# Kernel optimization log

Measured on AMD Instinct MI355X. Metric: run time of the kernel, lower is better.

Reference implementation:

```python
import jax, jax.numpy as jnp
import numpy as np

B = 128          # batch of trees (same topology)
N_LEAVES = 512
N_NODES = 2 * N_LEAVES - 1   # 1023, null child slot = N_NODES
IN_DIM = 300
MEM_DIM = 300


def _build_tree():
    # complete binary tree, level order: leaves first, then parents.
    null = N_NODES
    left = [null] * N_LEAVES
    right = [null] * N_LEAVES
    prev = list(range(N_LEAVES))
    nid = N_LEAVES
    while len(prev) > 1:
        cur = []
        for k in range(0, len(prev), 2):
            left.append(prev[k]); right.append(prev[k + 1])
            cur.append(nid); nid += 1
        prev = cur
    left = np.asarray(left, np.int32)
    right = np.asarray(right, np.int32)
    leaf_mask = (left == null).astype(np.int32)
    return left, right, leaf_mask


def setup_inputs() -> dict:
    key = jax.random.key(0)
    ks = jax.random.split(key, 5)
    left, right, leaf_mask = _build_tree()
    s = 0.05  # keep gates out of saturation
    return {
        "inputs": jax.random.normal(ks[0], (B, N_NODES, IN_DIM), jnp.float32),
        "Wfioux": jax.random.normal(ks[1], (IN_DIM, 4 * MEM_DIM), jnp.float32) * s,
        "b_fioux": jax.random.normal(ks[2], (4 * MEM_DIM,), jnp.float32) * s,
        "Wiouh": jax.random.normal(ks[3], (2 * MEM_DIM, 3 * MEM_DIM), jnp.float32) * s,
        "Wfh": jax.random.normal(ks[4], (2 * MEM_DIM, 2 * MEM_DIM), jnp.float32) * s,
        "left_idx": jnp.asarray(left),
        "right_idx": jnp.asarray(right),
        "leaf_mask": jnp.asarray(leaf_mask),
    }


def _tree_lstm(inputs, Wfioux, b_fioux, Wiouh, Wfh, left_idx, right_idx, leaf_mask):
    b, n, _ = inputs.shape
    mem = Wiouh.shape[1] // 3
    # internal nodes get zero input (as in the torch code)
    x = inputs * leaf_mask.astype(inputs.dtype)[None, :, None]
    # input-dependent gates precomputed for all nodes: [n, b, 4*mem]
    fioux = jnp.einsum('bni,io->nbo', x, Wfioux) + b_fioux

    C0 = jnp.zeros((n + 1, b, mem), inputs.dtype)  # row n = null child = zeros
    H0 = jnp.zeros((n + 1, b, mem), inputs.dtype)

    def step(carry, xs):
        C, H = carry
        i, li, ri, fioux_i = xs
        ch_c = jnp.concatenate([C[li], C[ri]], axis=-1)  # [b, 2*mem]
        ch_h = jnp.concatenate([H[li], H[ri]], axis=-1)
        fx, ix, ox, ux = jnp.split(fioux_i, 4, axis=-1)
        ih, oh, uh = jnp.split(ch_h @ Wiouh, 3, axis=-1)
        i_g = jax.nn.sigmoid(ix + ih)
        o_g = jax.nn.sigmoid(ox + oh)
        u_g = jnp.tanh(ux + uh)
        f_g = jax.nn.sigmoid(jnp.tile(fx, (1, 2)) + ch_h @ Wfh)
        fc = (f_g * ch_c).reshape(b, 2, mem).sum(axis=1)
        c = i_g * u_g + fc
        h = o_g * jnp.tanh(c)
        return (C.at[li * 0 + i].set(c), H.at[i].set(h)), None

    xs = (jnp.arange(n, dtype=jnp.int32), left_idx, right_idx, fioux)
    (C, H), _ = jax.lax.scan(step, (C0, H0), xs)
    return C[n - 1], H[n - 1]  # root state (c, h), each [b, mem]


def reference(inputs, Wfioux, b_fioux, Wiouh, Wfh, left_idx, right_idx, leaf_mask):
    return _tree_lstm(inputs, Wfioux, b_fioux, Wiouh, Wfh, left_idx, right_idx, leaf_mask)
```

## Files before the change

### kernel.cpp

```cpp
#include <hip/hip_runtime.h>
#include <cstdint>

#define BATCH 128
#define NODES 1023
#define LEAVES 512
#define IN_DIM 300
#define MEM 300
#define NP 320
#define OUT_HALF (BATCH*MEM)

typedef __bf16   bf16x8 __attribute__((ext_vector_type(8)));
typedef short    s16x8  __attribute__((ext_vector_type(8)));
typedef short    s16x4  __attribute__((ext_vector_type(4)));
typedef float    f32x4  __attribute__((ext_vector_type(4)));
typedef _Float16 half_t;

__device__ __forceinline__ short f2bf(float f) {
    unsigned u = __float_as_uint(f);
    u += 0x7fff + ((u >> 16) & 1);
    return (short)(u >> 16);
}
__device__ __forceinline__ float sigf(float x)  { return 1.0f / (1.0f + __expf(-x)); }
__device__ __forceinline__ float tanhf_(float x){ return 1.0f - 2.0f / (1.0f + __expf(2.0f * x)); }

__device__ __forceinline__ f32x4 mfma16(s16x8 a, s16x8 b, f32x4 c) {
    return __builtin_amdgcn_mfma_f32_16x16x32_bf16(
        __builtin_bit_cast(bf16x8, a), __builtin_bit_cast(bf16x8, b), c, 0, 0, 0);
}

__device__ __forceinline__ void dma16(const short* src, short* ldsBase) {
    __builtin_amdgcn_global_load_lds(
        (const __attribute__((address_space(1))) unsigned int*)src,
        (__attribute__((address_space(3))) unsigned int*)ldsBase,
        16, 0, 0);
}

__global__ __launch_bounds__(256) void pack_node_w(
    const float* __restrict__ Wiouh, const float* __restrict__ Wfh, short* __restrict__ Wpk)
{
    int gid = blockIdx.x * 256 + threadIdx.x;
    if (gid >= 2000 * 64) return;
    int fb = gid >> 6, l = gid & 63;
    int kb = fb / 100, rem = fb % 100, s = rem / 20, nb = rem % 20;
    int n = nb * 16 + (l & 15);
    int kbase = kb * 32 + (l >> 4) * 8;
    short v[8];
#pragma unroll
    for (int j = 0; j < 8; ++j) {
        int kp = kbase + j;
        int side = kp >= NP;
        int kk = kp - side * NP;
        float f = 0.0f;
        if (kk < MEM && n < MEM) {
            int k = side * MEM + kk;
            f = (s < 3) ? Wiouh[(size_t)k * 900 + s * 300 + n]
                        : Wfh[(size_t)k * 600 + (s - 3) * 300 + n];
        }
        v[j] = f2bf(f);
    }
    *(s16x8*)&Wpk[(size_t)gid * 8] = *(s16x8*)v;
}

__global__ __launch_bounds__(256) void pack_leaf_w(
    const float* __restrict__ Wfioux, short* __restrict__ Wpk)
{
    int gid = blockIdx.x * 256 + threadIdx.x;
    if (gid >= 600 * 64) return;
    int fb = gid >> 6, l = gid & 63;
    int kb = fb / 60, rem = fb % 60, s = rem / 20, nb = rem % 20;
    int n = nb * 16 + (l & 15);
    int kbase = kb * 32 + (l >> 4) * 8;
    short v[8];
#pragma unroll
    for (int j = 0; j < 8; ++j) {
        int kp = kbase + j;
        float f = 0.0f;
        if (kp < IN_DIM && n < MEM)
            f = Wfioux[(size_t)kp * 1200 + (s + 1) * 300 + n];
        v[j] = f2bf(f);
    }
    *(s16x8*)&Wpk[(size_t)gid * 8] = *(s16x8*)v;
}

__global__ __launch_bounds__(256) void pack_x(
    const float* __restrict__ inputs, short* __restrict__ X)
{
    int gid = blockIdx.x * 256 + threadIdx.x;
    if (gid >= LEAVES * BATCH * (NP / 4)) return;
    int q = gid % (NP / 4);
    int rb = gid / (NP / 4);
    int b = rb % BATCH, leaf = rb / BATCH;
    short v[4] = {0, 0, 0, 0};
    if (q < IN_DIM / 4) {
        f32x4 f = *(const f32x4*)&inputs[((size_t)b * NODES + leaf) * IN_DIM + q * 4];
        v[0] = f2bf(f[0]); v[1] = f2bf(f[1]); v[2] = f2bf(f[2]); v[3] = f2bf(f[3]);
    }
    *(s16x4*)&X[(size_t)gid * 4] = *(s16x4*)v;
}

__global__ __launch_bounds__(256, 3) void leaf_mfma(
    const short* __restrict__ X, const short* __restrict__ Wpk,
    const float* __restrict__ b_fioux, half_t* __restrict__ C, short* __restrict__ H)
{
    __shared__ short Bs[12 * 512];
    const int t = threadIdx.x;
    const int l = t & 63, w = t >> 6;
    const int lane16 = l & 15, quad = l >> 4;
    const int leaf = blockIdx.x;
    const int y = blockIdx.y;

    const short* Xb = X + (size_t)leaf * BATCH * NP;

    f32x4 acc[3][4][2];
#pragma unroll
    for (int s = 0; s < 3; ++s)
#pragma unroll
        for (int f = 0; f < 4; ++f)
#pragma unroll
            for (int mi = 0; mi < 2; ++mi) acc[s][f][mi] = (f32x4)(0.0f);

    for (int kb = 0; kb < 10; ++kb) {
        const int koff = kb * 32 + quad * 8;
#pragma unroll
        for (int fl = w; fl < 12; fl += 4) {
            int s = fl >> 2, f = fl & 3;
            const short* src = Wpk + ((size_t)((kb * 3 + s) * 20 + y * 4 + f) * 64 + l) * 8;
            dma16(src, &Bs[fl * 512]);
        }
        s16x8 a[2];
        a[0] = *(const s16x8*)(Xb + (size_t)(w * 32 + lane16) * NP + koff);
        a[1] = *(const s16x8*)(Xb + (size_t)(w * 32 + 16 + lane16) * NP + koff);
        __syncthreads();
#pragma unroll
        for (int s = 0; s < 3; ++s)
#pragma unroll
            for (int f = 0; f < 4; ++f) {
                s16x8 b = *(const s16x8*)&Bs[(s * 4 + f) * 512 + l * 8];
                acc[s][f][0] = mfma16(a[0], b, acc[s][f][0]);
                acc[s][f][1] = mfma16(a[1], b, acc[s][f][1]);
            }
        __syncthreads();
    }

#pragma unroll
    for (int f = 0; f < 4; ++f) {
        const int col = y * 64 + f * 16 + lane16;
        const bool valid = col < MEM;
        float bi = 0, bo = 0, bu = 0;
        if (valid) { bi = b_fioux[300 + col]; bo = b_fioux[600 + col]; bu = b_fioux[900 + col]; }
#pragma unroll
        for (int mi = 0; mi < 2; ++mi)
#pragma unroll
            for (int r = 0; r < 4; ++r) {
                int b = w * 32 + mi * 16 + quad * 4 + r;
                size_t hIdx = ((size_t)leaf * BATCH + b) * NP + col;
                if (valid) {
                    float ig = sigf(acc[0][f][mi][r] + bi);
                    float og = sigf(acc[1][f][mi][r] + bo);
                    float ug = tanhf_(acc[2][f][mi][r] + bu);
                    float c = ig * ug;
                    float h = og * tanhf_(c);
                    C[((size_t)leaf * BATCH + b) * MEM + col] = (half_t)c;
                    H[hIdx] = f2bf(h);
                } else {
                    H[hIdx] = 0;
                }
            }
    }
}

__global__ __launch_bounds__(256, 3) void node_mfma(
    const short* __restrict__ Wpk, const float* __restrict__ b_fioux,
    const int* __restrict__ left_idx, const int* __restrict__ right_idx,
    half_t* __restrict__ C, short* __restrict__ H,
    int level_start, float* __restrict__ out)
{
    __shared__ short Bs[10 * 512];
    const int t = threadIdx.x;
    const int l = t & 63, w = t >> 6;
    const int lane16 = l & 15, quad = l >> 4;
    const int node = level_start + blockIdx.x;
    const int y = blockIdx.y;

    const int li = left_idx[node], ri = right_idx[node];
    const short* HL = H + (size_t)li * BATCH * NP;
    const short* HR = H + (size_t)ri * BATCH * NP;

    f32x4 acc[5][2][2];
#pragma unroll
    for (int s = 0; s < 5; ++s)
#pragma unroll
        for (int f = 0; f < 2; ++f)
#pragma unroll
            for (int mi = 0; mi < 2; ++mi) acc[s][f][mi] = (f32x4)(0.0f);

    for (int kb = 0; kb < 20; ++kb) {
        const int side = kb >= 10;
        const int koff = (kb - side * 10) * 32 + quad * 8;
        const short* Hb = (side ? HR : HL) + koff;
#pragma unroll
        for (int fl = w; fl < 10; fl += 4) {
            int s = fl >> 1, f = fl & 1;
            const short* src = Wpk + ((size_t)((kb * 5 + s) * 20 + y * 2 + f) * 64 + l) * 8;
            dma16(src, &Bs[fl * 512]);
        }
        s16x8 a[2];
        a[0] = *(const s16x8*)(Hb + (size_t)(w * 32 + lane16) * NP);
        a[1] = *(const s16x8*)(Hb + (size_t)(w * 32 + 16 + lane16) * NP);
        __syncthreads();
#pragma unroll
        for (int s = 0; s < 5; ++s)
#pragma unroll
            for (int f = 0; f < 2; ++f) {
                s16x8 b = *(const s16x8*)&Bs[(s * 2 + f) * 512 + l * 8];
                acc[s][f][0] = mfma16(a[0], b, acc[s][f][0]);
                acc[s][f][1] = mfma16(a[1], b, acc[s][f][1]);
            }
        __syncthreads();
    }

#pragma unroll
    for (int f = 0; f < 2; ++f) {
        const int col = y * 32 + f * 16 + lane16;
        const bool valid = col < MEM;
        float bff = 0, bi = 0, bo = 0, bu = 0;
        if (valid) {
            bff = b_fioux[col]; bi = b_fioux[300 + col];
            bo = b_fioux[600 + col]; bu = b_fioux[900 + col];
        }
#pragma unroll
        for (int mi = 0; mi < 2; ++mi)
#pragma unroll
            for (int r = 0; r < 4; ++r) {
                int row = w * 32 + mi * 16 + quad * 4 + r;
                size_t hIdx = ((size_t)node * BATCH + row) * NP + col;
                if (valid) {
                    float cl = (float)C[((size_t)li * BATCH + row) * MEM + col];
                    float cr = (float)C[((size_t)ri * BATCH + row) * MEM + col];
                    float ig = sigf(acc[0][f][mi][r] + bi);
                    float og = sigf(acc[1][f][mi][r] + bo);
                    float ug = tanhf_(acc[2][f][mi][r] + bu);
                    float fl = sigf(acc[3][f][mi][r] + bff);
                    float fr = sigf(acc[4][f][mi][r] + bff);
                    float c = ig * ug + fl * cl + fr * cr;
                    float h = og * tanhf_(c);
                    C[((size_t)node * BATCH + row) * MEM + col] = (half_t)c;
                    H[hIdx] = f2bf(h);
                    if (out) {
                        out[row * MEM + col] = c;
                        out[OUT_HALF + row * MEM + col] = h;
                    }
                } else {
                    H[hIdx] = 0;
                }
            }
    }
}

extern "C" void kernel_launch(void* const* d_in, const int* in_sizes, int n_in,
                              void* d_out, int out_size, void* d_ws, size_t ws_size,
                              hipStream_t stream) {
    const float* inputs  = (const float*)d_in[0];
    const float* Wfioux  = (const float*)d_in[1];
    const float* b_fioux = (const float*)d_in[2];
    const float* Wiouh   = (const float*)d_in[3];
    const float* Wfh     = (const float*)d_in[4];
    const int*   left_idx  = (const int*)d_in[5];
    const int*   right_idx = (const int*)d_in[6];

    half_t* C   = (half_t*)d_ws;
    short*  H   = (short*)(C + (size_t)NODES * BATCH * MEM);
    short* WpkN = H + (size_t)NODES * BATCH * NP;
    short* WpkL = WpkN + (size_t)2000 * 512;
    short* X    = WpkL + (size_t)600 * 512;
    float* out  = (float*)d_out;

    pack_x<<<(LEAVES * BATCH * (NP / 4) + 255) / 256, 256, 0, stream>>>(inputs, X);
    pack_leaf_w<<<150, 256, 0, stream>>>(Wfioux, WpkL);
    pack_node_w<<<500, 256, 0, stream>>>(Wiouh, Wfh, WpkN);

    leaf_mfma<<<dim3(LEAVES, 5), 256, 0, stream>>>(X, WpkL, b_fioux, C, H);

    static const int starts[9] = {512, 768, 896, 960, 992, 1008, 1016, 1020, 1022};
    static const int sizes [9] = {256, 128,  64,  32,  16,    8,    4,    2,    1};
    for (int lvl = 0; lvl < 9; ++lvl) {
        bool root = (lvl == 8);
        node_mfma<<<dim3(sizes[lvl], 10), 256, 0, stream>>>(
            WpkN, b_fioux, left_idx, right_idx, C, H, starts[lvl],
            root ? out : nullptr);
    }
}
```

Before: 697.9 us.

## Double-buffer weight tiles and prefetch activations in leaf and node MFMA kernels

Both the leaf and internal-node GEMM kernels now ping-pong between two LDS buffers, issuing the DMA for the next K-block of packed weights and the register load of the next activation fragment before running the MFMAs on the current block. This removes one of the two barriers per iteration and overlaps global memory latency with matrix math. The node kernel also processes two 32-wide K sub-blocks per stage, halving the number of stages and barriers. The cost is more LDS (node kernel grows from 10 KB to 40 KB) and more live registers, which may cut occupancy under the 3-blocks launch bound.

```diff
diff --git a/kernel.cpp b/kernel.cpp
--- a/kernel.cpp
+++ b/kernel.cpp
@@ -102,7 +102,7 @@
     const short* __restrict__ X, const short* __restrict__ Wpk,
     const float* __restrict__ b_fioux, half_t* __restrict__ C, short* __restrict__ H)
 {
-    __shared__ short Bs[12 * 512];
+    __shared__ short Bs[2][12 * 512];
     const int t = threadIdx.x;
     const int l = t & 63, w = t >> 6;
     const int lane16 = l & 15, quad = l >> 4;
@@ -119,27 +119,39 @@
 #pragma unroll
             for (int mi = 0; mi < 2; ++mi) acc[s][f][mi] = (f32x4)(0.0f);
 
-    for (int kb = 0; kb < 10; ++kb) {
-        const int koff = kb * 32 + quad * 8;
+    auto stage = [&](int kb, int buf) {
 #pragma unroll
         for (int fl = w; fl < 12; fl += 4) {
             int s = fl >> 2, f = fl & 3;
             const short* src = Wpk + ((size_t)((kb * 3 + s) * 20 + y * 4 + f) * 64 + l) * 8;
-            dma16(src, &Bs[fl * 512]);
-        }
-        s16x8 a[2];
+            dma16(src, &Bs[buf][fl * 512]);
+        }
+    };
+    auto aload = [&](int kb, s16x8 (&a)[2]) {
+        const int koff = kb * 32 + quad * 8;
         a[0] = *(const s16x8*)(Xb + (size_t)(w * 32 + lane16) * NP + koff);
         a[1] = *(const s16x8*)(Xb + (size_t)(w * 32 + 16 + lane16) * NP + koff);
-        __syncthreads();
+    };
+
+    s16x8 aC[2], aN[2];
+    stage(0, 0);
+    aload(0, aC);
+    __syncthreads();
+
+#pragma unroll
+    for (int kb = 0; kb < 10; ++kb) {
+        const int buf = kb & 1;
+        if (kb < 9) { stage(kb + 1, buf ^ 1); aload(kb + 1, aN); }
 #pragma unroll
         for (int s = 0; s < 3; ++s)
 #pragma unroll
             for (int f = 0; f < 4; ++f) {
-                s16x8 b = *(const s16x8*)&Bs[(s * 4 + f) * 512 + l * 8];
-                acc[s][f][0] = mfma16(a[0], b, acc[s][f][0]);
-                acc[s][f][1] = mfma16(a[1], b, acc[s][f][1]);
+                s16x8 b = *(const s16x8*)&Bs[buf][(s * 4 + f) * 512 + l * 8];
+                acc[s][f][0] = mfma16(aC[0], b, acc[s][f][0]);
+                acc[s][f][1] = mfma16(aC[1], b, acc[s][f][1]);
             }
         __syncthreads();
+        aC[0] = aN[0]; aC[1] = aN[1];
     }
 
 #pragma unroll
@@ -175,7 +187,7 @@
     half_t* __restrict__ C, short* __restrict__ H,
     int level_start, float* __restrict__ out)
 {
-    __shared__ short Bs[10 * 512];
+    __shared__ short Bs[2][20 * 512];
     const int t = threadIdx.x;
     const int l = t & 63, w = t >> 6;
     const int lane16 = l & 15, quad = l >> 4;
@@ -194,29 +206,48 @@
 #pragma unroll
             for (int mi = 0; mi < 2; ++mi) acc[s][f][mi] = (f32x4)(0.0f);
 
-    for (int kb = 0; kb < 20; ++kb) {
-        const int side = kb >= 10;
-        const int koff = (kb - side * 10) * 32 + quad * 8;
-        const short* Hb = (side ? HR : HL) + koff;
-#pragma unroll
-        for (int fl = w; fl < 10; fl += 4) {
-            int s = fl >> 1, f = fl & 1;
-            const short* src = Wpk + ((size_t)((kb * 5 + s) * 20 + y * 2 + f) * 64 + l) * 8;
-            dma16(src, &Bs[fl * 512]);
-        }
-        s16x8 a[2];
-        a[0] = *(const s16x8*)(Hb + (size_t)(w * 32 + lane16) * NP);
-        a[1] = *(const s16x8*)(Hb + (size_t)(w * 32 + 16 + lane16) * NP);
+    auto stage = [&](int st, int buf) {
+#pragma unroll
+        for (int fl = w; fl < 20; fl += 4) {
+            int ksub = fl / 10, rem = fl - ksub * 10;
+            int s = rem >> 1, f = rem & 1;
+            int kb32 = st * 2 + ksub;
+            const short* src = Wpk + ((size_t)((kb32 * 5 + s) * 20 + y * 2 + f) * 64 + l) * 8;
+            dma16(src, &Bs[buf][fl * 512]);
+        }
+    };
+    auto aload = [&](int st, s16x8 (&a)[2][2]) {
+        const int side = st >= 5;
+        const short* Hb = (side ? HR : HL) + (st - side * 5) * 64 + quad * 8;
+#pragma unroll
+        for (int ksub = 0; ksub < 2; ++ksub) {
+            a[ksub][0] = *(const s16x8*)(Hb + (size_t)(w * 32 + lane16) * NP + ksub * 32);
+            a[ksub][1] = *(const s16x8*)(Hb + (size_t)(w * 32 + 16 + lane16) * NP + ksub * 32);
+        }
+    };
+
+    s16x8 aC[2][2], aN[2][2];
+    stage(0, 0);
+    aload(0, aC);
+    __syncthreads();
+
+#pragma unroll
+    for (int st = 0; st < 10; ++st) {
+        const int buf = st & 1;
+        if (st < 9) { stage(st + 1, buf ^ 1); aload(st + 1, aN); }
+#pragma unroll
+        for (int ksub = 0; ksub < 2; ++ksub)
+#pragma unroll
+            for (int s = 0; s < 5; ++s)
+#pragma unroll
+                for (int f = 0; f < 2; ++f) {
+                    s16x8 b = *(const s16x8*)&Bs[buf][(ksub * 10 + s * 2 + f) * 512 + l * 8];
+                    acc[s][f][0] = mfma16(aC[ksub][0], b, acc[s][f][0]);
+                    acc[s][f][1] = mfma16(aC[ksub][1], b, acc[s][f][1]);
+                }
         __syncthreads();
 #pragma unroll
-        for (int s = 0; s < 5; ++s)
-#pragma unroll
-            for (int f = 0; f < 2; ++f) {
-                s16x8 b = *(const s16x8*)&Bs[(s * 2 + f) * 512 + l * 8];
-                acc[s][f][0] = mfma16(a[0], b, acc[s][f][0]);
-                acc[s][f][1] = mfma16(a[1], b, acc[s][f][1]);
-            }
-        __syncthreads();
+        for (int i = 0; i < 2; ++i) { aC[i][0] = aN[i][0]; aC[i][1] = aN[i][1]; }
     }
 
 #pragma unroll
```

Measured after the change: 705.6 us. Within noise of the previous version (+1.1%).

## Software-pipeline K loop with 4-stage LDS ring and prefetch distance three

Applied to the files above, without the earlier changes.

Both the leaf and node MFMA kernels replace their synchronous per-k-block load/compute loop with a fully unrolled pipeline. It uses four LDS buffers and keeps weight DMAs and A-fragment loads three stages ahead, waiting with explicit vmcnt counts and a single barrier per step. The aim is to hide global-memory latency behind MFMA work instead of stalling on two barriers each iteration. In exchange it uses four times the shared memory (48KB per block) and more registers for the A fragments, which may cut occupancy under launch_bounds(256,3). The node kernel also pads its DMA to 12 slots so the vmcnt counts match, which adds duplicate loads. Dropping the trailing barrier relies on the 4-deep ring to avoid overwriting a buffer that is still being read.

```diff
diff --git a/kernel.cpp b/kernel.cpp
--- a/kernel.cpp
+++ b/kernel.cpp
@@ -102,7 +102,7 @@
     const short* __restrict__ X, const short* __restrict__ Wpk,
     const float* __restrict__ b_fioux, half_t* __restrict__ C, short* __restrict__ H)
 {
-    __shared__ short Bs[12 * 512];
+    __shared__ short Bs[4][12 * 512];
     const int t = threadIdx.x;
     const int l = t & 63, w = t >> 6;
     const int lane16 = l & 15, quad = l >> 4;
@@ -119,28 +119,49 @@
 #pragma unroll
             for (int mi = 0; mi < 2; ++mi) acc[s][f][mi] = (f32x4)(0.0f);
 
-    for (int kb = 0; kb < 10; ++kb) {
-        const int koff = kb * 32 + quad * 8;
-#pragma unroll
-        for (int fl = w; fl < 12; fl += 4) {
-            int s = fl >> 2, f = fl & 3;
-            const short* src = Wpk + ((size_t)((kb * 3 + s) * 20 + y * 4 + f) * 64 + l) * 8;
-            dma16(src, &Bs[fl * 512]);
-        }
-        s16x8 a[2];
-        a[0] = *(const s16x8*)(Xb + (size_t)(w * 32 + lane16) * NP + koff);
-        a[1] = *(const s16x8*)(Xb + (size_t)(w * 32 + 16 + lane16) * NP + koff);
-        __syncthreads();
-#pragma unroll
-        for (int s = 0; s < 3; ++s)
-#pragma unroll
-            for (int f = 0; f < 4; ++f) {
-                s16x8 b = *(const s16x8*)&Bs[(s * 4 + f) * 512 + l * 8];
-                acc[s][f][0] = mfma16(a[0], b, acc[s][f][0]);
-                acc[s][f][1] = mfma16(a[1], b, acc[s][f][1]);
-            }
-        __syncthreads();
-    }
+    s16x8 A[4][2];
+
+#define L_STAGE(KB, BUF) do {                                                    \
+    _Pragma("unroll")                                                            \
+    for (int fl = w; fl < 12; fl += 4) {                                         \
+        int s_ = fl >> 2, f_ = fl & 3;                                           \
+        const short* src_ = Wpk +                                                \
+            ((size_t)(((KB) * 3 + s_) * 20 + y * 4 + f_) * 64 + l) * 8;          \
+        dma16(src_, &Bs[BUF][fl * 512]);                                         \
+    } } while (0)
+
+#define L_ALOAD(KB, SLOT) do {                                                   \
+    const int koff_ = (KB) * 32 + quad * 8;                                      \
+    A[SLOT][0] = *(const s16x8*)(Xb + (size_t)(w * 32 + lane16) * NP + koff_);   \
+    A[SLOT][1] = *(const s16x8*)(Xb + (size_t)(w * 32 + 16 + lane16) * NP + koff_); \
+} while (0)
+
+    L_STAGE(0, 0); L_ALOAD(0, 0);
+    L_STAGE(1, 1); L_ALOAD(1, 1);
+    L_STAGE(2, 2); L_ALOAD(2, 2);
+
+#define L_STEP(ST, WAITN) do {                                                   \
+    asm volatile("s_waitcnt vmcnt(" #WAITN ")" ::: "memory");                    \
+    __builtin_amdgcn_s_barrier();                                                \
+    asm volatile("" ::: "memory");                                               \
+    if ((ST) + 3 < 10) { L_STAGE((ST) + 3, ((ST) + 3) & 3);                      \
+                         L_ALOAD((ST) + 3, ((ST) + 3) & 3); }                    \
+    _Pragma("unroll")                                                            \
+    for (int s_ = 0; s_ < 3; ++s_) {                                             \
+        _Pragma("unroll")                                                        \
+        for (int f_ = 0; f_ < 4; ++f_) {                                         \
+            s16x8 b_ = *(const s16x8*)&Bs[(ST) & 3][(s_ * 4 + f_) * 512 + l * 8];\
+            acc[s_][f_][0] = mfma16(A[(ST) & 3][0], b_, acc[s_][f_][0]);         \
+            acc[s_][f_][1] = mfma16(A[(ST) & 3][1], b_, acc[s_][f_][1]);         \
+        }                                                                        \
+    } } while (0)
+
+    L_STEP(0, 10); L_STEP(1, 10); L_STEP(2, 10); L_STEP(3, 10); L_STEP(4, 10);
+    L_STEP(5, 10); L_STEP(6, 10); L_STEP(7, 10); L_STEP(8, 5);  L_STEP(9, 0);
+
+#undef L_STEP
+#undef L_ALOAD
+#undef L_STAGE
 
 #pragma unroll
     for (int f = 0; f < 4; ++f) {
@@ -175,7 +196,7 @@
     half_t* __restrict__ C, short* __restrict__ H,
     int level_start, float* __restrict__ out)
 {
-    __shared__ short Bs[10 * 512];
+    __shared__ short Bs[4][12 * 512];
     const int t = threadIdx.x;
     const int l = t & 63, w = t >> 6;
     const int lane16 = l & 15, quad = l >> 4;
@@ -194,30 +215,53 @@
 #pragma unroll
             for (int mi = 0; mi < 2; ++mi) acc[s][f][mi] = (f32x4)(0.0f);
 
-    for (int kb = 0; kb < 20; ++kb) {
-        const int side = kb >= 10;
-        const int koff = (kb - side * 10) * 32 + quad * 8;
-        const short* Hb = (side ? HR : HL) + koff;
-#pragma unroll
-        for (int fl = w; fl < 10; fl += 4) {
-            int s = fl >> 1, f = fl & 1;
-            const short* src = Wpk + ((size_t)((kb * 5 + s) * 20 + y * 2 + f) * 64 + l) * 8;
-            dma16(src, &Bs[fl * 512]);
-        }
-        s16x8 a[2];
-        a[0] = *(const s16x8*)(Hb + (size_t)(w * 32 + lane16) * NP);
-        a[1] = *(const s16x8*)(Hb + (size_t)(w * 32 + 16 + lane16) * NP);
-        __syncthreads();
-#pragma unroll
-        for (int s = 0; s < 5; ++s)
-#pragma unroll
-            for (int f = 0; f < 2; ++f) {
-                s16x8 b = *(const s16x8*)&Bs[(s * 2 + f) * 512 + l * 8];
-                acc[s][f][0] = mfma16(a[0], b, acc[s][f][0]);
-                acc[s][f][1] = mfma16(a[1], b, acc[s][f][1]);
-            }
-        __syncthreads();
-    }
+    s16x8 A[4][2];
+
+#define N_STAGE(KB, BUF) do {                                                    \
+    _Pragma("unroll")                                                            \
+    for (int fl = w; fl < 12; fl += 4) {                                         \
+        int rfl_ = (fl < 10) ? fl : fl - 10;               \
+        int s_ = rfl_ >> 1, f_ = rfl_ & 1;                                       \
+        const short* src_ = Wpk +                                                \
+            ((size_t)(((KB) * 5 + s_) * 20 + y * 2 + f_) * 64 + l) * 8;          \
+        dma16(src_, &Bs[BUF][fl * 512]);                                         \
+    } } while (0)
+
+#define N_ALOAD(KB, SLOT) do {                                                   \
+    const short* Hb_ = (((KB) >= 10) ? HR : HL) +                                \
+                       ((KB) - (((KB) >= 10) ? 10 : 0)) * 32 + quad * 8;         \
+    A[SLOT][0] = *(const s16x8*)(Hb_ + (size_t)(w * 32 + lane16) * NP);          \
+    A[SLOT][1] = *(const s16x8*)(Hb_ + (size_t)(w * 32 + 16 + lane16) * NP);     \
+} while (0)
+
+    N_STAGE(0, 0); N_ALOAD(0, 0);
+    N_STAGE(1, 1); N_ALOAD(1, 1);
+    N_STAGE(2, 2); N_ALOAD(2, 2);
+
+#define N_STEP(ST, WAITN) do {                                                   \
+    asm volatile("s_waitcnt vmcnt(" #WAITN ")" ::: "memory");                    \
+    __builtin_amdgcn_s_barrier();                                                \
+    asm volatile("" ::: "memory");                                               \
+    if ((ST) + 3 < 20) { N_STAGE((ST) + 3, ((ST) + 3) & 3);                      \
+                         N_ALOAD((ST) + 3, ((ST) + 3) & 3); }                    \
+    _Pragma("unroll")                                                            \
+    for (int s_ = 0; s_ < 5; ++s_) {                                             \
+        _Pragma("unroll")                                                        \
+        for (int f_ = 0; f_ < 2; ++f_) {                                         \
+            s16x8 b_ = *(const s16x8*)&Bs[(ST) & 3][(s_ * 2 + f_) * 512 + l * 8];\
+            acc[s_][f_][0] = mfma16(A[(ST) & 3][0], b_, acc[s_][f_][0]);         \
+            acc[s_][f_][1] = mfma16(A[(ST) & 3][1], b_, acc[s_][f_][1]);         \
+        }                                                                        \
+    } } while (0)
+
+    N_STEP(0, 10);  N_STEP(1, 10);  N_STEP(2, 10);  N_STEP(3, 10);  N_STEP(4, 10);
+    N_STEP(5, 10);  N_STEP(6, 10);  N_STEP(7, 10);  N_STEP(8, 10);  N_STEP(9, 10);
+    N_STEP(10, 10); N_STEP(11, 10); N_STEP(12, 10); N_STEP(13, 10); N_STEP(14, 10);
+    N_STEP(15, 10); N_STEP(16, 10); N_STEP(17, 10); N_STEP(18, 5);  N_STEP(19, 0);
+
+#undef N_STEP
+#undef N_ALOAD
+#undef N_STAGE
 
 #pragma unroll
     for (int f = 0; f < 2; ++f) {
```

Result: faster. 654.6 us (-6.2%).
